# Performance work log

Measured on AMD Instinct MI355X. Metric: run time of the kernel, lower is better.

Reference implementation:

```python
import jax, jax.numpy as jnp
import numpy as np

B = 1024
P = 8
D = 2048
NUM_IDS = 64
MARGIN = 0.3
EPS = 1e-12


def setup_inputs() -> dict:
    key = jax.random.key(0)
    k1, k2, k3 = jax.random.split(key, 3)
    feats = jax.random.normal(k1, (B, P * D), dtype=jnp.float32)
    labels = jax.random.randint(k2, (B,), 0, NUM_IDS, dtype=jnp.int64)
    subs = jax.random.randint(k3, (B,), 0, 2, dtype=jnp.int64)
    return {"feats": feats, "labels": labels, "subs": subs}


def reference(feats, labels, subs):
    b = feats.shape[0]
    f = feats.reshape(b, -1, D)  # [B, P, D]
    dt = f.dtype

    # Per-sample class centers via a single segment-mean pass
    # (equivalent to the original per-sample boolean-mask mean loop).
    seg_sum = jax.ops.segment_sum(f, labels, num_segments=NUM_IDS)  # [NUM_IDS, P, D]
    counts = jax.ops.segment_sum(jnp.ones((b,), dt), labels, num_segments=NUM_IDS)
    centers_by_id = seg_sum / jnp.maximum(counts, 1.0)[:, None, None]
    centers = centers_by_id[labels]  # [B, P, D]

    # dist_ap[i] = sum_p ||f[i,p] - center[i,p]||
    d_ap = jnp.sqrt(jnp.clip(jnp.sum((f - centers) ** 2, axis=-1), EPS, None)).sum(-1)  # [B]
    dist_ap = d_ap[:, None] + d_ap[None, :]  # [B, B]

    # pairwise_distance: dist_aa[i,j] = sum_p ||f[i,p] - f[j,p]||, via gemm trick
    sq = jnp.sum(f * f, axis=-1)  # [B, P]
    inner = jnp.einsum('ipd,jpd->ijp', f, f)  # [B, B, P]
    d2 = sq[:, None, :] + sq[None, :, :] - 2.0 * inner
    dist_aa = jnp.sqrt(jnp.clip(d2, EPS, None)).sum(-1)  # [B, B]

    # masked margin loss over negative (different-label) pairs
    mask = labels[:, None] != labels[None, :]  # [B, B] bool
    vals = jnp.clip(dist_ap - dist_aa + MARGIN, 0.0, None)
    maskf = mask.astype(dt)
    loss = jnp.sum(vals * maskf) / jnp.sum(maskf)
    return loss
```

## Files before the change

### kernel.cpp

```cpp
#include <hip/hip_runtime.h>
#include <hip/hip_bf16.h>

#define B_ 1024
#define P_ 8
#define D_ 2048
#define FD_ (P_ * D_)
#define NID 64
#define MARGIN_ 0.3f
#define EPS_ 1e-12f

typedef unsigned short u16;
typedef short short8_t __attribute__((ext_vector_type(8)));
typedef float float4_t __attribute__((ext_vector_type(4)));

#define AS1 __attribute__((address_space(1)))
#define AS3 __attribute__((address_space(3)))

__device__ __forceinline__ float bf2f(u16 v) {
    unsigned x = (unsigned)v << 16;
    float f;
    __builtin_memcpy(&f, &x, 4);
    return f;
}

static const size_t OFF_COUNTS  = 0;
static const size_t OFF_OFFS    = 256;
static const size_t OFF_PERM    = 512;
static const size_t OFF_NEG     = 4608;
static const size_t OFF_POS     = 4624;
static const size_t OFF_SQ      = 65536;
static const size_t OFF_DAP     = 98304;
static const size_t OFF_CENTERS = 131072;
static const size_t OFF_FB      = OFF_CENTERS + 4194304;
static const size_t OFF_PD      = OFF_FB + (size_t)B_ * FD_ * 2;

__global__ void k_counts(const int* __restrict__ labels, float* countsf, int* offs,
                         int* perm, float* negcnt) {
    __shared__ int h[NID], o[NID], cur[NID];
    int tid = threadIdx.x;
    if (tid < NID) h[tid] = 0;
    __syncthreads();
    for (int i = tid; i < B_; i += 256) atomicAdd(&h[labels[i]], 1);
    __syncthreads();
    if (tid == 0) {
        int acc = 0;
        long long ss = 0;
        for (int c = 0; c < NID; c++) {
            o[c] = acc;
            acc += h[c];
            ss += (long long)h[c] * h[c];
        }
        *negcnt = (float)((long long)B_ * B_ - ss);
    }
    __syncthreads();
    if (tid < NID) {
        countsf[tid] = (float)h[tid];
        offs[tid] = o[tid];
        cur[tid] = o[tid];
    }
    __syncthreads();
    for (int i = tid; i < B_; i += 256) {
        int pos = atomicAdd(&cur[labels[i]], 1);
        perm[pos] = i;
    }
}

__global__ void k_centers(const float* __restrict__ feats, const int* __restrict__ offs,
                          const int* __restrict__ perm, const float* __restrict__ countsf,
                          float* __restrict__ centers) {
    int cls = blockIdx.x >> 3;
    int ch  = blockIdx.x & 7;
    int base = ch * 2048 + threadIdx.x * 4;
    float a0 = 0.f, a1 = 0.f, a2 = 0.f, a3 = 0.f;
    float b0 = 0.f, b1 = 0.f, b2 = 0.f, b3 = 0.f;
    int off = offs[cls];
    int cnt = (int)countsf[cls];
    for (int m = 0; m < cnt; m++) {
        const float* row = feats + (size_t)perm[off + m] * FD_ + base;
        float4 f0 = *(const float4*)(row);
        float4 f1 = *(const float4*)(row + 1024);
        a0 += f0.x; a1 += f0.y; a2 += f0.z; a3 += f0.w;
        b0 += f1.x; b1 += f1.y; b2 += f1.z; b3 += f1.w;
    }
    float inv = 1.0f / fmaxf((float)cnt, 1.0f);
    float* crow = centers + (size_t)cls * FD_ + base;
    float4 o0 = {a0 * inv, a1 * inv, a2 * inv, a3 * inv};
    float4 o1 = {b0 * inv, b1 * inv, b2 * inv, b3 * inv};
    *(float4*)(crow) = o0;
    *(float4*)(crow + 1024) = o1;
}

__global__ void k_rowstats(const float* __restrict__ feats, const int* __restrict__ labels,
                           const float* __restrict__ centers, __hip_bfloat16* __restrict__ fb,
                           float* __restrict__ sq, float* __restrict__ dap) {
    int i = blockIdx.x;
    int tid = threadIdx.x;
    int w = tid >> 6, lane = tid & 63;
    int lab = labels[i];
    const float* frow = feats + (size_t)i * FD_;
    const float* crow = centers + (size_t)lab * FD_;
    u16* brow = (u16*)(fb + (size_t)i * FD_);
    __shared__ float dsum[4];
    float dacc = 0.f;
#pragma unroll
    for (int pp = 0; pp < 2; pp++) {
        int p = w * 2 + pp;
        int off = p * D_;
        float s2 = 0.f, sc = 0.f;
#pragma unroll
        for (int ch = 0; ch < 8; ch++) {
            int d = off + ch * 256 + lane * 4;
            float4 f = *(const float4*)(frow + d);
            float4 c = *(const float4*)(crow + d);
            ushort4 b;
            b.x = __bfloat16_as_ushort(__float2bfloat16(f.x));
            b.y = __bfloat16_as_ushort(__float2bfloat16(f.y));
            b.z = __bfloat16_as_ushort(__float2bfloat16(f.z));
            b.w = __bfloat16_as_ushort(__float2bfloat16(f.w));
            *(ushort4*)(brow + d) = b;
            s2 += f.x * f.x + f.y * f.y + f.z * f.z + f.w * f.w;
            float dx = f.x - c.x, dy = f.y - c.y, dz = f.z - c.z, dw = f.w - c.w;
            sc += dx * dx + dy * dy + dz * dz + dw * dw;
        }
        for (int o = 32; o; o >>= 1) {
            s2 += __shfl_down(s2, o, 64);
            sc += __shfl_down(sc, o, 64);
        }
        if (lane == 0) {
            sq[i * P_ + p] = s2;
            dacc += sqrtf(fmaxf(sc, EPS_));
        }
    }
    if (lane == 0) dsum[w] = dacc;
    __syncthreads();
    if (tid == 0) dap[i] = dsum[0] + dsum[1] + dsum[2] + dsum[3];
}

__global__ __launch_bounds__(512, 4) void k_pairs(const u16* __restrict__ fb,
                                                  const float* __restrict__ sq,
                                                  u16* __restrict__ pd) {
    const int i0 = blockIdx.y * 128, j0 = blockIdx.x * 128;
    const int p = blockIdx.z;
    __shared__ u16 smem[32768];
    __shared__ float sqAs[128], sqBs[128];
    const int tid = threadIdx.x;
    const int lane = tid & 63, wid = tid >> 6;
    const int s = wid & 3, h = wid >> 2;
    if (tid < 128) sqAs[tid] = sq[(i0 + tid) * 8 + p];
    else if (tid < 256) sqBs[tid - 128] = sq[(j0 + tid - 128) * 8 + p];

    const int wi = (s >> 1) * 64, wj = (s & 1) * 64;
    const int lhi = lane >> 4, llo = lane & 15;
    const int sl = llo & 7;
    const int lr = lane >> 3;
    const int lc = (lane & 7) ^ lr;

    u16* const As = &smem[h * 8192];
    u16* const Bs = &smem[16384 + h * 8192];

    const size_t colbase = (size_t)p * D_ + (size_t)h * 1024 + (size_t)lc * 8;
    const u16* gA[4];
    const u16* gB[4];
    u16* lA[4];
    u16* lB[4];
#pragma unroll
    for (int inst = 0; inst < 4; inst++) {
        int r0 = s * 32 + inst * 8;
        gA[inst] = fb + (size_t)(i0 + r0 + lr) * FD_ + colbase;
        gB[inst] = fb + (size_t)(j0 + r0 + lr) * FD_ + colbase;
        lA[inst] = As + r0 * 64;
        lB[inst] = Bs + r0 * 64;
    }

    float4_t acc[4][4];
#pragma unroll
    for (int a = 0; a < 4; a++)
#pragma unroll
        for (int b = 0; b < 4; b++) acc[a][b] = (float4_t){0.f, 0.f, 0.f, 0.f};

    for (int kb = 0; kb < 16; kb++) {
        const int koff = kb * 64;
        __syncthreads();
#pragma unroll
        for (int inst = 0; inst < 4; inst++) {
            __builtin_amdgcn_global_load_lds((const AS1 void*)(gA[inst] + koff),
                                             (AS3 void*)lA[inst], 16, 0, 0);
            __builtin_amdgcn_global_load_lds((const AS1 void*)(gB[inst] + koff),
                                             (AS3 void*)lB[inst], 16, 0, 0);
        }
        __syncthreads();
#pragma unroll
        for (int ks = 0; ks < 2; ks++) {
            const int pc = ((ks * 4 + lhi) ^ sl) * 8;
            short8_t af[4], bf[4];
#pragma unroll
            for (int a = 0; a < 4; a++) {
                af[a] = *(const short8_t*)(&As[(wi + a * 16 + llo) * 64 + pc]);
                bf[a] = *(const short8_t*)(&Bs[(wj + a * 16 + llo) * 64 + pc]);
            }
#pragma unroll
            for (int a = 0; a < 4; a++)
#pragma unroll
                for (int b = 0; b < 4; b++)
                    acc[a][b] = __builtin_amdgcn_mfma_f32_16x16x32_bf16(
                        af[a], bf[b], acc[a][b], 0, 0, 0);
        }
    }
    __syncthreads();
    float* ep = (float*)smem;
    if (h == 1) {
#pragma unroll
        for (int a = 0; a < 4; a++)
#pragma unroll
            for (int b = 0; b < 4; b++)
                *(float4_t*)&ep[(((s * 4 + a) * 4 + b) * 64 + lane) * 4] = acc[a][b];
    }
    __syncthreads();
    if (h == 0) {
        u16* outp = pd + (size_t)p * B_ * B_;
#pragma unroll
        for (int a = 0; a < 4; a++)
#pragma unroll
            for (int b = 0; b < 4; b++) {
                float4_t o = *(const float4_t*)&ep[(((s * 4 + a) * 4 + b) * 64 + lane) * 4];
#pragma unroll
                for (int r = 0; r < 4; r++) {
                    int il = wi + a * 16 + lhi * 4 + r;
                    int jl = wj + b * 16 + llo;
                    float t = acc[a][b][r] + o[r];
                    float d2 = sqAs[il] + sqBs[jl] - 2.0f * t;
                    float v = sqrtf(fmaxf(d2, EPS_));
                    outp[(size_t)(i0 + il) * B_ + (j0 + jl)] =
                        __bfloat16_as_ushort(__float2bfloat16(v));
                }
            }
    }
}

__global__ void k_lossred(const u16* __restrict__ pd, const float* __restrict__ dap,
                          const int* __restrict__ labels, float* possum) {
    int i = blockIdx.x;
    int tid = threadIdx.x;
    float di = dap[i];
    int li = labels[i];
    float lsum = 0.f;
    for (int j = tid; j < B_; j += 256) {
        if (labels[j] != li) {
            float daa = 0.f;
#pragma unroll
            for (int p = 0; p < P_; p++)
                daa += bf2f(pd[(size_t)p * B_ * B_ + (size_t)i * B_ + j]);
            float v = di + dap[j] - daa + MARGIN_;
            lsum += fmaxf(v, 0.f);
        }
    }
    for (int o = 32; o; o >>= 1) lsum += __shfl_down(lsum, o, 64);
    __shared__ float red[4];
    int wid = tid >> 6, lane = tid & 63;
    if (lane == 0) red[wid] = lsum;
    __syncthreads();
    if (tid == 0) atomicAdd(possum, red[0] + red[1] + red[2] + red[3]);
}

__global__ void k_finalize(const float* possum, const float* negcnt, float* out) {
    out[0] = possum[0] / negcnt[0];
}

extern "C" void kernel_launch(void* const* d_in, const int* in_sizes, int n_in,
                              void* d_out, int out_size, void* d_ws, size_t ws_size,
                              hipStream_t stream) {
    const float* feats = (const float*)d_in[0];
    const int* labels  = (const int*)d_in[1];
    float* out = (float*)d_out;

    char* w = (char*)d_ws;
    float* countsf = (float*)(w + OFF_COUNTS);
    int* offs      = (int*)(w + OFF_OFFS);
    int* perm      = (int*)(w + OFF_PERM);
    float* negcnt  = (float*)(w + OFF_NEG);
    float* possum  = (float*)(w + OFF_POS);
    float* sq      = (float*)(w + OFF_SQ);
    float* dap     = (float*)(w + OFF_DAP);
    float* centers = (float*)(w + OFF_CENTERS);
    __hip_bfloat16* fb = (__hip_bfloat16*)(w + OFF_FB);
    u16* pd        = (u16*)(w + OFF_PD);

    hipMemsetAsync(w + OFF_POS, 0, 4, stream);

    k_counts<<<1, 256, 0, stream>>>(labels, countsf, offs, perm, negcnt);
    k_centers<<<512, 256, 0, stream>>>(feats, offs, perm, countsf, centers);
    k_rowstats<<<B_, 256, 0, stream>>>(feats, labels, centers, fb, sq, dap);
    k_pairs<<<dim3(8, 8, 8), 512, 0, stream>>>((const u16*)fb, sq, pd);
    k_lossred<<<B_, 256, 0, stream>>>(pd, dap, labels, possum);
    k_finalize<<<1, 1, 0, stream>>>(possum, negcnt, out);
}
```

Measured before the change: 193.3 us.

## Switch pairwise GEMM to FP8 and derive anchor-center distances from Gram sums

Result: faster. 169.5 us (-12.3%).

```diff
diff --git a/kernel.cpp b/kernel.cpp
--- a/kernel.cpp
+++ b/kernel.cpp
@@ -10,7 +10,6 @@
 #define EPS_ 1e-12f
 
 typedef unsigned short u16;
-typedef short short8_t __attribute__((ext_vector_type(8)));
 typedef float float4_t __attribute__((ext_vector_type(4)));
 
 #define AS1 __attribute__((address_space(1)))
@@ -23,16 +22,16 @@
     return f;
 }
 
-static const size_t OFF_COUNTS  = 0;
-static const size_t OFF_OFFS    = 256;
-static const size_t OFF_PERM    = 512;
-static const size_t OFF_NEG     = 4608;
-static const size_t OFF_POS     = 4624;
-static const size_t OFF_SQ      = 65536;
-static const size_t OFF_DAP     = 98304;
-static const size_t OFF_CENTERS = 131072;
-static const size_t OFF_FB      = OFF_CENTERS + 4194304;
-static const size_t OFF_PD      = OFF_FB + (size_t)B_ * FD_ * 2;
+static const size_t OFF_COUNTS = 0;
+static const size_t OFF_OFFS   = 256;
+static const size_t OFF_PERM   = 512;
+static const size_t OFF_NEG    = 4608;
+static const size_t OFF_POS    = 8176;
+static const size_t OFF_S      = 8192;
+static const size_t OFF_SQ     = 40960;
+static const size_t OFF_DAP    = 73728;
+static const size_t OFF_FB     = 131072;
+static const size_t OFF_PD     = OFF_FB + (size_t)B_ * FD_;
 
 __global__ void k_counts(const int* __restrict__ labels, float* countsf, int* offs,
                          int* perm, float* negcnt) {
@@ -65,89 +64,53 @@
     }
 }
 
-__global__ void k_centers(const float* __restrict__ feats, const int* __restrict__ offs,
-                          const int* __restrict__ perm, const float* __restrict__ countsf,
-                          float* __restrict__ centers) {
-    int cls = blockIdx.x >> 3;
-    int ch  = blockIdx.x & 7;
-    int base = ch * 2048 + threadIdx.x * 4;
-    float a0 = 0.f, a1 = 0.f, a2 = 0.f, a3 = 0.f;
-    float b0 = 0.f, b1 = 0.f, b2 = 0.f, b3 = 0.f;
-    int off = offs[cls];
-    int cnt = (int)countsf[cls];
-    for (int m = 0; m < cnt; m++) {
-        const float* row = feats + (size_t)perm[off + m] * FD_ + base;
-        float4 f0 = *(const float4*)(row);
-        float4 f1 = *(const float4*)(row + 1024);
-        a0 += f0.x; a1 += f0.y; a2 += f0.z; a3 += f0.w;
-        b0 += f1.x; b1 += f1.y; b2 += f1.z; b3 += f1.w;
-    }
-    float inv = 1.0f / fmaxf((float)cnt, 1.0f);
-    float* crow = centers + (size_t)cls * FD_ + base;
-    float4 o0 = {a0 * inv, a1 * inv, a2 * inv, a3 * inv};
-    float4 o1 = {b0 * inv, b1 * inv, b2 * inv, b3 * inv};
-    *(float4*)(crow) = o0;
-    *(float4*)(crow + 1024) = o1;
-}
-
-__global__ void k_rowstats(const float* __restrict__ feats, const int* __restrict__ labels,
-                           const float* __restrict__ centers, __hip_bfloat16* __restrict__ fb,
-                           float* __restrict__ sq, float* __restrict__ dap) {
+__global__ void k_rowstats(const float* __restrict__ feats, unsigned char* __restrict__ fb,
+                           float* __restrict__ sq) {
     int i = blockIdx.x;
     int tid = threadIdx.x;
     int w = tid >> 6, lane = tid & 63;
-    int lab = labels[i];
     const float* frow = feats + (size_t)i * FD_;
-    const float* crow = centers + (size_t)lab * FD_;
-    u16* brow = (u16*)(fb + (size_t)i * FD_);
-    __shared__ float dsum[4];
-    float dacc = 0.f;
+    unsigned char* brow = fb + (size_t)i * FD_;
 #pragma unroll
     for (int pp = 0; pp < 2; pp++) {
         int p = w * 2 + pp;
         int off = p * D_;
-        float s2 = 0.f, sc = 0.f;
+        float s2 = 0.f;
 #pragma unroll
         for (int ch = 0; ch < 8; ch++) {
             int d = off + ch * 256 + lane * 4;
             float4 f = *(const float4*)(frow + d);
-            float4 c = *(const float4*)(crow + d);
-            ushort4 b;
-            b.x = __bfloat16_as_ushort(__float2bfloat16(f.x));
-            b.y = __bfloat16_as_ushort(__float2bfloat16(f.y));
-            b.z = __bfloat16_as_ushort(__float2bfloat16(f.z));
-            b.w = __bfloat16_as_ushort(__float2bfloat16(f.w));
-            *(ushort4*)(brow + d) = b;
+            int pk = __builtin_amdgcn_cvt_pk_fp8_f32(f.x, f.y, 0, false);
+            pk = __builtin_amdgcn_cvt_pk_fp8_f32(f.z, f.w, pk, true);
+            *(unsigned int*)(brow + d) = (unsigned int)pk;
             s2 += f.x * f.x + f.y * f.y + f.z * f.z + f.w * f.w;
-            float dx = f.x - c.x, dy = f.y - c.y, dz = f.z - c.z, dw = f.w - c.w;
-            sc += dx * dx + dy * dy + dz * dz + dw * dw;
-        }
-        for (int o = 32; o; o >>= 1) {
-            s2 += __shfl_down(s2, o, 64);
-            sc += __shfl_down(sc, o, 64);
-        }
-        if (lane == 0) {
-            sq[i * P_ + p] = s2;
-            dacc += sqrtf(fmaxf(sc, EPS_));
-        }
-    }
-    if (lane == 0) dsum[w] = dacc;
-    __syncthreads();
-    if (tid == 0) dap[i] = dsum[0] + dsum[1] + dsum[2] + dsum[3];
-}
-
-__global__ __launch_bounds__(512, 4) void k_pairs(const u16* __restrict__ fb,
+        }
+        for (int o = 32; o; o >>= 1) s2 += __shfl_down(s2, o, 64);
+        if (lane == 0) sq[i * P_ + p] = s2;
+    }
+}
+
+__global__ __launch_bounds__(512, 4) void k_pairs(const unsigned char* __restrict__ fb,
                                                   const float* __restrict__ sq,
+                                                  const int* __restrict__ labels,
+                                                  float* __restrict__ S,
                                                   u16* __restrict__ pd) {
     const int i0 = blockIdx.y * 128, j0 = blockIdx.x * 128;
     const int p = blockIdx.z;
-    __shared__ u16 smem[32768];
+    __shared__ __align__(16) unsigned char smem[65536];
     __shared__ float sqAs[128], sqBs[128];
+    __shared__ int labA[128], labB[128];
     const int tid = threadIdx.x;
     const int lane = tid & 63, wid = tid >> 6;
     const int s = wid & 3, h = wid >> 2;
-    if (tid < 128) sqAs[tid] = sq[(i0 + tid) * 8 + p];
-    else if (tid < 256) sqBs[tid - 128] = sq[(j0 + tid - 128) * 8 + p];
+    if (tid < 128) {
+        sqAs[tid] = sq[(i0 + tid) * 8 + p];
+        labA[tid] = labels[i0 + tid];
+    } else if (tid < 256) {
+        int t = tid - 128;
+        sqBs[t] = sq[(j0 + t) * 8 + p];
+        labB[t] = labels[j0 + t];
+    }
 
     const int wi = (s >> 1) * 64, wj = (s & 1) * 64;
     const int lhi = lane >> 4, llo = lane & 15;
@@ -155,21 +118,21 @@
     const int lr = lane >> 3;
     const int lc = (lane & 7) ^ lr;
 
-    u16* const As = &smem[h * 8192];
-    u16* const Bs = &smem[16384 + h * 8192];
-
-    const size_t colbase = (size_t)p * D_ + (size_t)h * 1024 + (size_t)lc * 8;
-    const u16* gA[4];
-    const u16* gB[4];
-    u16* lA[4];
-    u16* lB[4];
+    unsigned char* const As = smem + h * 16384;
+    unsigned char* const Bs = smem + 32768 + h * 16384;
+
+    const size_t colbase = (size_t)p * D_ + (size_t)h * 1024 + (size_t)lc * 16;
+    const unsigned char* gA[4];
+    const unsigned char* gB[4];
+    unsigned char* lA[4];
+    unsigned char* lB[4];
 #pragma unroll
     for (int inst = 0; inst < 4; inst++) {
         int r0 = s * 32 + inst * 8;
         gA[inst] = fb + (size_t)(i0 + r0 + lr) * FD_ + colbase;
         gB[inst] = fb + (size_t)(j0 + r0 + lr) * FD_ + colbase;
-        lA[inst] = As + r0 * 64;
-        lB[inst] = Bs + r0 * 64;
+        lA[inst] = As + r0 * 128;
+        lB[inst] = Bs + r0 * 128;
     }
 
     float4_t acc[4][4];
@@ -178,8 +141,8 @@
 #pragma unroll
         for (int b = 0; b < 4; b++) acc[a][b] = (float4_t){0.f, 0.f, 0.f, 0.f};
 
-    for (int kb = 0; kb < 16; kb++) {
-        const int koff = kb * 64;
+    for (int kb = 0; kb < 8; kb++) {
+        const int koff = kb * 128;
         __syncthreads();
 #pragma unroll
         for (int inst = 0; inst < 4; inst++) {
@@ -190,19 +153,19 @@
         }
         __syncthreads();
 #pragma unroll
-        for (int ks = 0; ks < 2; ks++) {
-            const int pc = ((ks * 4 + lhi) ^ sl) * 8;
-            short8_t af[4], bf[4];
+        for (int ks = 0; ks < 4; ks++) {
+            const int pcb = ((2 * ks + (lhi >> 1)) ^ sl) * 16 + (lhi & 1) * 8;
+            long af[4], bf[4];
 #pragma unroll
             for (int a = 0; a < 4; a++) {
-                af[a] = *(const short8_t*)(&As[(wi + a * 16 + llo) * 64 + pc]);
-                bf[a] = *(const short8_t*)(&Bs[(wj + a * 16 + llo) * 64 + pc]);
+                af[a] = *(const long*)(As + (wi + a * 16 + llo) * 128 + pcb);
+                bf[a] = *(const long*)(Bs + (wj + a * 16 + llo) * 128 + pcb);
             }
 #pragma unroll
             for (int a = 0; a < 4; a++)
 #pragma unroll
                 for (int b = 0; b < 4; b++)
-                    acc[a][b] = __builtin_amdgcn_mfma_f32_16x16x32_bf16(
+                    acc[a][b] = __builtin_amdgcn_mfma_f32_16x16x32_fp8_fp8(
                         af[a], bf[b], acc[a][b], 0, 0, 0);
         }
     }
@@ -218,22 +181,74 @@
     __syncthreads();
     if (h == 0) {
         u16* outp = pd + (size_t)p * B_ * B_;
+        float rs[4][4];
 #pragma unroll
         for (int a = 0; a < 4; a++)
+#pragma unroll
+            for (int r = 0; r < 4; r++) rs[a][r] = 0.f;
+#pragma unroll
+        for (int a = 0; a < 4; a++) {
+            int la0 = labA[wi + a * 16 + lhi * 4 + 0];
+            int la1 = labA[wi + a * 16 + lhi * 4 + 1];
+            int la2 = labA[wi + a * 16 + lhi * 4 + 2];
+            int la3 = labA[wi + a * 16 + lhi * 4 + 3];
 #pragma unroll
             for (int b = 0; b < 4; b++) {
                 float4_t o = *(const float4_t*)&ep[(((s * 4 + a) * 4 + b) * 64 + lane) * 4];
+                int lb = labB[wj + b * 16 + llo];
+                int jl = wj + b * 16 + llo;
 #pragma unroll
                 for (int r = 0; r < 4; r++) {
                     int il = wi + a * 16 + lhi * 4 + r;
-                    int jl = wj + b * 16 + llo;
                     float t = acc[a][b][r] + o[r];
                     float d2 = sqAs[il] + sqBs[jl] - 2.0f * t;
-                    float v = sqrtf(fmaxf(d2, EPS_));
                     outp[(size_t)(i0 + il) * B_ + (j0 + jl)] =
-                        __bfloat16_as_ushort(__float2bfloat16(v));
+                        __bfloat16_as_ushort(__float2bfloat16(sqrtf(fmaxf(d2, EPS_))));
+                    int la = (r == 0) ? la0 : (r == 1) ? la1 : (r == 2) ? la2 : la3;
+                    if (lb == la) rs[a][r] += t;
                 }
             }
+        }
+#pragma unroll
+        for (int a = 0; a < 4; a++)
+#pragma unroll
+            for (int r = 0; r < 4; r++) {
+                float v = rs[a][r];
+                v += __shfl_xor(v, 1, 64);
+                v += __shfl_xor(v, 2, 64);
+                v += __shfl_xor(v, 4, 64);
+                v += __shfl_xor(v, 8, 64);
+                if (llo == 0)
+                    atomicAdd(&S[(size_t)(i0 + wi + a * 16 + lhi * 4 + r) * 8 + p], v);
+            }
+    }
+}
+
+__global__ void k_dap(const float* __restrict__ S, const float* __restrict__ sq,
+                      const float* __restrict__ countsf, const int* __restrict__ offs,
+                      const int* __restrict__ perm, float* __restrict__ dap) {
+    int c = blockIdx.x;
+    int tid = threadIdx.x;
+    int cnt = (int)countsf[c];
+    int off = offs[c];
+    __shared__ float T[8];
+    if (tid < 8) {
+        float t = 0.f;
+        for (int m = 0; m < cnt; m++) t += S[(size_t)perm[off + m] * 8 + tid];
+        T[tid] = t;
+    }
+    __syncthreads();
+    float n = fmaxf((float)cnt, 1.f);
+    float inv = 1.f / n, inv2 = inv * inv;
+    for (int m = tid; m < cnt; m += 64) {
+        int i = perm[off + m];
+        float d = 0.f;
+#pragma unroll
+        for (int p = 0; p < 8; p++) {
+            float d2 = sq[i * 8 + p] - 2.f * inv * S[(size_t)i * 8 + p] + inv2 * T[p];
+            d += sqrtf(fmaxf(d2, EPS_));
+        }
+        dap[i] = d;
     }
 }
 
@@ -279,18 +294,18 @@
     int* perm      = (int*)(w + OFF_PERM);
     float* negcnt  = (float*)(w + OFF_NEG);
     float* possum  = (float*)(w + OFF_POS);
+    float* S       = (float*)(w + OFF_S);
     float* sq      = (float*)(w + OFF_SQ);
     float* dap     = (float*)(w + OFF_DAP);
-    float* centers = (float*)(w + OFF_CENTERS);
-    __hip_bfloat16* fb = (__hip_bfloat16*)(w + OFF_FB);
+    unsigned char* fb = (unsigned char*)(w + OFF_FB);
     u16* pd        = (u16*)(w + OFF_PD);
 
-    hipMemsetAsync(w + OFF_POS, 0, 4, stream);
+    hipMemsetAsync(w + OFF_POS, 0, (OFF_S - OFF_POS) + (size_t)B_ * P_ * 4, stream);
 
     k_counts<<<1, 256, 0, stream>>>(labels, countsf, offs, perm, negcnt);
-    k_centers<<<512, 256, 0, stream>>>(feats, offs, perm, countsf, centers);
-    k_rowstats<<<B_, 256, 0, stream>>>(feats, labels, centers, fb, sq, dap);
-    k_pairs<<<dim3(8, 8, 8), 512, 0, stream>>>((const u16*)fb, sq, pd);
+    k_rowstats<<<B_, 256, 0, stream>>>(feats, fb, sq);
+    k_pairs<<<dim3(8, 8, 8), 512, 0, stream>>>(fb, sq, labels, S, pd);
+    k_dap<<<NID, 64, 0, stream>>>(S, sq, countsf, offs, perm, dap);
     k_lossred<<<B_, 256, 0, stream>>>(pd, dap, labels, possum);
     k_finalize<<<1, 1, 0, stream>>>(possum, negcnt, out);
 }
```
